# Kernel tuning notes

Hardware: AMD Instinct MI355X
Metric: run time of the kernel (lower is better)

## Reference

```python
import jax, jax.numpy as jnp
import numpy as np

B, D, E, G, P, H = 8192, 2048, 8, 4, 512, 192
T, DT, TAU, VTH, VRESET = 20, 0.001, 0.02, 0.5, 0.0
DELTA0, KTOP, KROUTE, PREDW = 7.0, 32, 2, 0.1


def setup_inputs() -> dict:
    key = jax.random.key(0)
    ks = jax.random.split(key, 12)
    s = 0.02
    return {
        "query_embedding": jax.random.normal(ks[0], (B, D), jnp.float32),
        "Wg": jax.random.normal(ks[1], (2, E), jnp.float32) * s,
        "bg": jnp.zeros((E,), jnp.float32),
        "Wp": jax.random.normal(ks[2], (2, E), jnp.float32) * s,
        "bp": jnp.zeros((E,), jnp.float32),
        "Wgg": jax.random.normal(ks[3], (2, G), jnp.float32) * s,
        "bgg": jnp.zeros((G,), jnp.float32),
        "W1": jax.random.normal(ks[4], (E, D, P), jnp.float32) * (1.0 / np.sqrt(D)),
        "b1": jnp.zeros((E, P), jnp.float32),
        "W2": jax.random.normal(ks[5], (E, P, D), jnp.float32) * (1.0 / np.sqrt(P)),
        "b2": jnp.zeros((E, D), jnp.float32),
    }


def reference(query_embedding, Wg, bg, Wp, bp, Wgg, bgg, W1, b1, W2, b2):
    x = query_embedding  # [B, D], already embed_dim -> no pad/slice
    dtype = x.dtype

    # --- Phasor bank temporal features on per-row mean ---
    qm = jnp.mean(x, axis=-1)  # [B]
    freqs = DELTA0 * jnp.arange(1, H + 1, dtype=dtype)  # [H]
    ang = qm[:, None] * freqs[None, :]  # [B, H]
    temporal = jnp.concatenate([jnp.cos(ang), jnp.sin(ang)], axis=-1)  # [B, 2H]

    # --- Spiking attention over top-K |x| indices (LIF over T steps) ---
    topk_idx = jax.lax.top_k(jnp.abs(x), KTOP)[1]  # [B, K]
    rows = jnp.arange(B)[:, None]
    I = jnp.zeros((B, D), dtype).at[rows, topk_idx].add(1.0)  # input current [B, vocab=D]

    def lif_step(v, _):
        v = v * (1.0 - DT / TAU) + I
        spike = (v >= VTH).astype(dtype)
        v = jnp.where(spike > 0, VRESET, v)
        return v, spike

    _, spikes = jax.lax.scan(lif_step, jnp.zeros((B, D), dtype), None, length=T)
    attention_gains = jnp.mean(spikes, axis=0)  # [B, D] spike rates

    # --- Bio gating inputs ---
    gate_in = jnp.stack([jnp.mean(temporal, axis=-1), jnp.mean(attention_gains, axis=-1)], axis=-1)  # [B, 2]

    gate_logits = gate_in @ Wg + bg  # [B, E]
    gate_logits = gate_logits - PREDW * (gate_in @ Wp + bp)

    # group routing bias: experts grouped round-robin i % G
    group_logits = gate_in @ Wgg + bgg  # [B, G]
    gmap = jax.nn.one_hot(jnp.arange(E) % G, G, dtype=dtype)  # [E, G]
    gate_logits = gate_logits + group_logits @ gmap.T

    gate_weights = jax.nn.softmax(gate_logits, axis=-1)  # temperature = 1

    # top-k routing + renormalization
    _, tidx = jax.lax.top_k(gate_weights, KROUTE)
    mask = jnp.zeros_like(gate_weights).at[rows, tidx].set(1.0)
    gated = gate_weights * mask
    gate_weights = gated / (jnp.sum(gated, axis=-1, keepdims=True) + 1e-9)

    # --- Dense MLP experts (bottleneck P = hidden // 4) ---
    h = jax.nn.relu(jnp.einsum('bd,edp->ebp', x, W1) + b1[:, None, :])  # [E, B, P]
    expert_out = jnp.einsum('ebp,eph->ebh', h, W2) + b2[:, None, :]  # [E, B, D]

    # gate-weighted combine
    context = jnp.einsum('be,ebh->bh', gate_weights, expert_out)  # [B, D]
    return context
```

## Files before the change

### kernel.cpp

```cpp
#include <hip/hip_runtime.h>
#include <stdint.h>

#define NB 8192
#define ND 2048
#define NE 8
#define NG 4
#define NP 512
#define NH 192

typedef _Float16 half_t;
typedef half_t f16x8 __attribute__((ext_vector_type(8)));
typedef float f32x4 __attribute__((ext_vector_type(4)));

__device__ __forceinline__ void gload16(const void* g, void* l) {
  __builtin_amdgcn_global_load_lds(
      (const __attribute__((address_space(1))) void*)g,
      (__attribute__((address_space(3))) void*)l, 16, 0, 0);
}

__global__ __launch_bounds__(256) void k_convert(
    const float* __restrict__ x, half_t* __restrict__ xh, double* __restrict__ qm)
{
  const int b = blockIdx.x;
  const int t = threadIdx.x;
  const float* xr = x + (size_t)b * ND;
  const float4 v0 = ((const float4*)xr)[t * 2];
  const float4 v1 = ((const float4*)xr)[t * 2 + 1];
  float f[8] = {v0.x, v0.y, v0.z, v0.w, v1.x, v1.y, v1.z, v1.w};
  double s = 0.0;
  __align__(16) half_t hb[8];
#pragma unroll
  for (int i = 0; i < 8; i++) { s += (double)f[i]; hb[i] = (half_t)f[i]; }
  *reinterpret_cast<int4*>(xh + (size_t)b * ND + t * 8) = *reinterpret_cast<const int4*>(hb);

#pragma unroll
  for (int m = 32; m >= 1; m >>= 1) s += __shfl_xor(s, m);
  __shared__ double part[4];
  if ((t & 63) == 0) part[t >> 6] = s;
  __syncthreads();
  if (t == 0) qm[b] = (part[0] + part[1] + part[2] + part[3]) / (double)ND;
}

__global__ __launch_bounds__(256) void k_gate(
    const double* __restrict__ qm,
    const float* __restrict__ Wg, const float* __restrict__ bg,
    const float* __restrict__ Wp, const float* __restrict__ bp,
    const float* __restrict__ Wgg, const float* __restrict__ bgg,
    int* __restrict__ e0a, int* __restrict__ e1a,
    float* __restrict__ w0a, float* __restrict__ w1a)
{
  const int wave = threadIdx.x >> 6;
  const int lane = threadIdx.x & 63;
  const int b = blockIdx.x * 4 + wave;
  const double q = qm[b];

  double part = 0.0;
#pragma unroll
  for (int i = 0; i < 3; i++) {
    int h = lane + i * 64;
    double ang = q * (7.0 * (double)(h + 1));
    part += cos(ang) + sin(ang);
  }
#pragma unroll
  for (int m = 32; m >= 1; m >>= 1) part += __shfl_xor(part, m);
  const double tm = part / (2.0 * (double)NH);
  const double gi1 = 32.0 / 2048.0;

  double lg = -1.0e300;
  if (lane < 8) {
    const int e = lane, g = e & 3;
    lg = tm * (double)Wg[e] + gi1 * (double)Wg[NE + e] + (double)bg[e];
    lg -= 0.1 * (tm * (double)Wp[e] + gi1 * (double)Wp[NE + e] + (double)bp[e]);
    lg += tm * (double)Wgg[g] + gi1 * (double)Wgg[NG + g] + (double)bgg[g];
  }
  double mx = lg;
#pragma unroll
  for (int m = 4; m >= 1; m >>= 1) mx = fmax(mx, __shfl_xor(mx, m));
  double pe = 0.0;
  if (lane < 8) pe = exp(lg - mx);
  double ps = pe;
#pragma unroll
  for (int m = 4; m >= 1; m >>= 1) ps += __shfl_xor(ps, m);

  double lgs[8], pes[8];
#pragma unroll
  for (int e = 0; e < 8; e++) { lgs[e] = __shfl(lg, e); pes[e] = __shfl(pe, e); }

  if (lane == 0) {
    int e0 = 0;
    for (int e = 1; e < NE; e++) if (lgs[e] > lgs[e0]) e0 = e;
    int e1 = (e0 == 0) ? 1 : 0;
    for (int e = 0; e < NE; e++) if (e != e0 && lgs[e] > lgs[e1]) e1 = e;
    const double p0 = pes[e0] / ps;
    const double p1 = pes[e1] / ps;
    const double den = p0 + p1 + 1e-9;
    e0a[b] = e0; e1a[b] = e1;
    w0a[b] = (float)(p0 / den);
    w1a[b] = (float)(p1 / den);
  }
}

__global__ __launch_bounds__(256) void k_bucket(
    const int* __restrict__ e0a, const int* __restrict__ e1a,
    const float* __restrict__ w0a, const float* __restrict__ w1a,
    int* __restrict__ rowl, float* __restrict__ wl, int* __restrict__ cnt,
    int* __restrict__ pos0a, int* __restrict__ pos1a,
    int* __restrict__ rowlp, int* __restrict__ cntp)
{
  const int t = threadIdx.x;
  const int r = blockIdx.x * 256 + t;
  __shared__ int hist[16], base[16], cursor[16];
  __shared__ int histp[64], basep[64], cursorp[64];
  if (t < 16) { hist[t] = 0; cursor[t] = 0; }
  if (t < 64) { histp[t] = 0; cursorp[t] = 0; }
  __syncthreads();

  const int e0 = e0a[r], e1 = e1a[r];
  const int p = e0 * 8 + e1;
  atomicAdd(&hist[e0], 1);
  atomicAdd(&hist[8 + e1], 1);
  atomicAdd(&histp[p], 1);
  __syncthreads();
  if (t < 16) base[t] = atomicAdd(&cnt[t], hist[t]);
  if (t < 64) basep[t] = atomicAdd(&cntp[t], histp[t]);
  __syncthreads();

  int p0 = atomicAdd(&cursor[e0], 1);
  int idx0 = base[e0] + p0;
  rowl[e0 * NB + idx0] = r;
  wl[e0 * NB + idx0] = w0a[r];
  pos0a[r] = idx0;

  int p1 = atomicAdd(&cursor[8 + e1], 1);
  int idx1 = base[8 + e1] + p1;
  rowl[(8 + e1) * NB + idx1] = r;
  wl[(8 + e1) * NB + idx1] = w1a[r];
  pos1a[r] = idx1;

  int pp = atomicAdd(&cursorp[p], 1);
  rowlp[p * NB + basep[p] + pp] = r;
}

__global__ __launch_bounds__(256) void k_cvt_w(
    const float* __restrict__ W1, const float* __restrict__ W2,
    half_t* __restrict__ w1t, half_t* __restrict__ w2t)
{
  const int which = blockIdx.y;
  const int R = which ? NP : ND;
  const int C = which ? ND : NP;
  const float* src = which ? W2 : W1;
  half_t* dst = which ? w2t : w1t;
  const int tiles_c = C >> 5;
  const int tiles_per_e = (R >> 6) * tiles_c;
  int id = blockIdx.x;
  int e = id / tiles_per_e;
  int rem = id - e * tiles_per_e;
  int tr = rem / tiles_c, tc = rem - tr * tiles_c;
  __shared__ float tile[64][33];
  const int t = threadIdx.x;

  const int lc = t & 31, lr = t >> 5;
  const float* s = src + (size_t)e * R * C + (size_t)(tr * 64) * C + tc * 32;
#pragma unroll
  for (int i = 0; i < 8; i++)
    tile[lr + i * 8][lc] = s[(size_t)(lr + i * 8) * C + lc];
  __syncthreads();

  const int n = t >> 3, kc = (t & 7) * 8;
  __align__(16) half_t hb[8];
#pragma unroll
  for (int j = 0; j < 8; j++) hb[j] = (half_t)tile[kc + j][n];
  half_t* d = dst + (size_t)e * R * C + (size_t)(tc * 32 + n) * R + tr * 64 + kc;
  *reinterpret_cast<int4*>(d) = *reinterpret_cast<const int4*>(hb);
}

__global__ void k_prefix(const int* __restrict__ cnt, const int* __restrict__ cntp,
                         int* __restrict__ pbase,
                         int* __restrict__ i16b, int* __restrict__ i16m, int* __restrict__ n16,
                         int* __restrict__ ipp, int* __restrict__ ipm, int* __restrict__ np)
{
  const int t = threadIdx.x;
  if (t == 0) {
    int c[16];
#pragma unroll
    for (int i = 0; i < 16; i++) c[i] = cnt[i];
    int s = 0;
#pragma unroll
    for (int i = 0; i < 16; i++) { pbase[i] = s; s += c[i]; }
    int k = 0;
    for (int b = 0; b < 16; b++)
      for (int m0 = 0; m0 < c[b]; m0 += 128) { i16b[k] = b; i16m[k] = m0; k++; }
    *n16 = k;
  } else if (t == 64) {
    int c[64];
#pragma unroll
    for (int i = 0; i < 64; i++) c[i] = cntp[i];
    int k = 0;
    for (int p = 0; p < 64; p++)
      for (int m0 = 0; m0 < c[p]; m0 += 128) { ipp[k] = p; ipm[k] = m0; k++; }
    *np = k;
  }
}

__global__ __launch_bounds__(256, 2) void k_gemm1(
    const half_t* __restrict__ xh, const half_t* __restrict__ w1t,
    const float* __restrict__ b1,
    const int* __restrict__ rowl, const float* __restrict__ wl,
    const int* __restrict__ cnt, const int* __restrict__ pbase,
    const int* __restrict__ i16b, const int* __restrict__ i16m,
    const int* __restrict__ n16, half_t* __restrict__ Hbuf)
{
  const int wi = blockIdx.y;
  if (wi >= *n16) return;
  const int bucket = i16b[wi];
  const int m0 = i16m[wi];
  const int count = cnt[bucket];
  const int e = bucket & 7;
  const int n0 = blockIdx.x * 256;
  const int t = threadIdx.x;

  __shared__ __align__(16) half_t As[3][128 * 32];
  __shared__ __align__(16) half_t Bs[3][256 * 32];
  __shared__ int rows_s[128];
  __shared__ float ws_s[128];

  if (t < 128) {
    int mi = m0 + t;
    int idx = bucket * NB + (mi < count ? mi : m0);
    rows_s[t] = rowl[idx];
    ws_s[t] = wl[idx];
  }
  __syncthreads();

  const int w = t >> 6, lane = t & 63;
  const int cA0 = (w * 2) * 64 + lane, cA1 = cA0 + 64;
  const int rA0 = cA0 >> 2, rA1 = cA1 >> 2;
  const int kA0 = ((cA0 & 3) ^ ((rA0 >> 1) & 3)) * 8;
  const int kA1 = ((cA1 & 3) ^ ((rA1 >> 1) & 3)) * 8;
  const half_t* gA0 = xh + (size_t)rows_s[rA0] * ND + kA0;
  const half_t* gA1 = xh + (size_t)rows_s[rA1] * ND + kA1;
  const half_t* w1te = w1t + (size_t)e * NP * ND;
  const int cB0 = (w * 4) * 64 + lane, cB1 = cB0 + 64, cB2 = cB0 + 128, cB3 = cB0 + 192;
  const int rB0 = cB0 >> 2, rB1 = cB1 >> 2, rB2 = cB2 >> 2, rB3 = cB3 >> 2;
  const half_t* gB0 = w1te + (size_t)(n0 + rB0) * ND + ((cB0 & 3) ^ ((rB0 >> 1) & 3)) * 8;
  const half_t* gB1 = w1te + (size_t)(n0 + rB1) * ND + ((cB1 & 3) ^ ((rB1 >> 1) & 3)) * 8;
  const half_t* gB2 = w1te + (size_t)(n0 + rB2) * ND + ((cB2 & 3) ^ ((rB2 >> 1) & 3)) * 8;
  const half_t* gB3 = w1te + (size_t)(n0 + rB3) * ND + ((cB3 & 3) ^ ((rB3 >> 1) & 3)) * 8;

  const int wr = w >> 1, wc = w & 1;
  const int lrow = lane & 15, lk = lane >> 4;
  const int lko = (lk ^ ((lrow >> 1) & 3)) * 8;

  f32x4 acc[4][8];
#pragma unroll
  for (int i = 0; i < 4; i++)
#pragma unroll
    for (int j = 0; j < 8; j++) {
      acc[i][j][0] = 0.f; acc[i][j][1] = 0.f; acc[i][j][2] = 0.f; acc[i][j][3] = 0.f;
    }

  auto stage = [&](int bi, int tt) {
    const int kk = tt * 32;
    half_t* la = &As[bi][w * 1024];
    gload16(gA0 + kk, la);
    gload16(gA1 + kk, la + 512);
    half_t* lb = &Bs[bi][w * 2048];
    gload16(gB0 + kk, lb);
    gload16(gB1 + kk, lb + 512);
    gload16(gB2 + kk, lb + 1024);
    gload16(gB3 + kk, lb + 1536);
  };
  auto compute = [&](int bi) {
    f16x8 af[4], bf[8];
#pragma unroll
    for (int i = 0; i < 4; i++)
      af[i] = *reinterpret_cast<const f16x8*>(&As[bi][(wr * 64 + i * 16 + lrow) * 32 + lko]);
#pragma unroll
    for (int n = 0; n < 8; n++)
      bf[n] = *reinterpret_cast<const f16x8*>(&Bs[bi][(wc * 128 + n * 16 + lrow) * 32 + lko]);
#pragma unroll
    for (int mi = 0; mi < 4; mi++)
#pragma unroll
      for (int ni = 0; ni < 8; ni++)
        acc[mi][ni] = __builtin_amdgcn_mfma_f32_16x16x32_f16(af[mi], bf[ni], acc[mi][ni], 0, 0, 0);
  };

  stage(0, 0);
  stage(1, 1);
  asm volatile("s_waitcnt vmcnt(6)" ::: "memory");
  __builtin_amdgcn_s_barrier();
  for (int t3 = 0; t3 < 60; t3 += 3) {
    stage(2, t3 + 2); compute(0);
    asm volatile("s_waitcnt vmcnt(6) lgkmcnt(0)" ::: "memory");
    __builtin_amdgcn_s_barrier();
    stage(0, t3 + 3); compute(1);
    asm volatile("s_waitcnt vmcnt(6) lgkmcnt(0)" ::: "memory");
    __builtin_amdgcn_s_barrier();
    stage(1, t3 + 4); compute(2);
    asm volatile("s_waitcnt vmcnt(6) lgkmcnt(0)" ::: "memory");
    __builtin_amdgcn_s_barrier();
  }
  stage(2, 62); compute(0);
  asm volatile("s_waitcnt vmcnt(6) lgkmcnt(0)" ::: "memory");
  __builtin_amdgcn_s_barrier();
  stage(0, 63); compute(1);
  asm volatile("s_waitcnt vmcnt(6) lgkmcnt(0)" ::: "memory");
  __builtin_amdgcn_s_barrier();
  compute(2);
  asm volatile("s_waitcnt vmcnt(0) lgkmcnt(0)" ::: "memory");
  __builtin_amdgcn_s_barrier();
  compute(0);

  const int pb = pbase[bucket];
#pragma unroll
  for (int mi = 0; mi < 4; mi++) {
#pragma unroll
    for (int i = 0; i < 4; i++) {
      int lm = wr * 64 + mi * 16 + lk * 4 + i;
      if (m0 + lm < count) {
        size_t prow = (size_t)(pb + m0 + lm) * NP;
        float wcoef = ws_s[lm];
#pragma unroll
        for (int ni = 0; ni < 8; ni++) {
          int col = n0 + wc * 128 + ni * 16 + lrow;
          float v = acc[mi][ni][i] + b1[e * NP + col];
          v = v > 0.f ? v : 0.f;
          Hbuf[prow + col] = (half_t)(v * wcoef);
        }
      }
    }
  }
}

__global__ __launch_bounds__(256) void k_gemm2p(
    const half_t* __restrict__ Hbuf, const half_t* __restrict__ w2t,
    const float* __restrict__ b2,
    const int* __restrict__ rowlp, const int* __restrict__ cntp,
    const int* __restrict__ pbase,
    const int* __restrict__ pos0a, const int* __restrict__ pos1a,
    const float* __restrict__ w0a, const float* __restrict__ w1a,
    const int* __restrict__ ipp, const int* __restrict__ ipm,
    const int* __restrict__ np, float* __restrict__ out)
{
  const int wi = blockIdx.y;
  if (wi >= *np) return;
  const int p = ipp[wi];
  const int m0 = ipm[wi];
  const int count = cntp[p];
  const int e0 = p >> 3, e1 = p & 7;
  const int n0 = blockIdx.x * 128;
  const int t = threadIdx.x;

  __shared__ __align__(16) half_t As[3][128 * 32];
  __shared__ __align__(16) half_t Bs[3][128 * 32];
  __shared__ int h0_s[128], h1_s[128], rs_s[128];
  __shared__ float w0_s[128], w1_s[128];

  if (t < 128) {
    int mi = m0 + t;
    int r = rowlp[p * NB + (mi < count ? mi : m0)];
    rs_s[t] = r;
    h0_s[t] = pbase[e0] + pos0a[r];
    h1_s[t] = pbase[8 + e1] + pos1a[r];
    w0_s[t] = w0a[r];
    w1_s[t] = w1a[r];
  }
  __syncthreads();

  const int w = t >> 6, lane = t & 63;
  const int c0 = w * 128 + lane, c1 = c0 + 64;
  const int row0 = c0 >> 2, ch0 = c0 & 3;
  const int row1 = c1 >> 2, ch1 = c1 & 3;
  const int sw0 = (row0 >> 1) & 3, sw1 = (row1 >> 1) & 3;
  const half_t* w2e0 = w2t + (size_t)e0 * ND * NP;
  const half_t* w2e1 = w2t + (size_t)e1 * ND * NP;
  const half_t* sa00 = Hbuf + (size_t)h0_s[row0] * NP + ((ch0 ^ sw0) * 8);
  const half_t* sa01 = Hbuf + (size_t)h0_s[row1] * NP + ((ch1 ^ sw1) * 8);
  const half_t* sa10 = Hbuf + (size_t)h1_s[row0] * NP + ((ch0 ^ sw0) * 8);
  const half_t* sa11 = Hbuf + (size_t)h1_s[row1] * NP + ((ch1 ^ sw1) * 8);
  const half_t* pB00 = w2e0 + (size_t)(n0 + row0) * NP + ((ch0 ^ sw0) * 8);
  const half_t* pB01 = w2e0 + (size_t)(n0 + row1) * NP + ((ch1 ^ sw1) * 8);
  const half_t* pB10 = w2e1 + (size_t)(n0 + row0) * NP + ((ch0 ^ sw0) * 8);
  const half_t* pB11 = w2e1 + (size_t)(n0 + row1) * NP + ((ch1 ^ sw1) * 8);

  const int wr = w >> 1, wc = w & 1;
  const int lrow = lane & 15, lk = lane >> 4;
  const int lko = (lk ^ ((lrow >> 1) & 3)) * 8;

  f32x4 acc[4][4];
#pragma unroll
  for (int i = 0; i < 4; i++)
#pragma unroll
    for (int j = 0; j < 4; j++) {
      acc[i][j][0] = 0.f; acc[i][j][1] = 0.f; acc[i][j][2] = 0.f; acc[i][j][3] = 0.f;
    }

  const int NT = 32;

  auto stage = [&](int bi, int tt) {
    const int kk = (tt & 15) * 32;
    half_t* la = &As[bi][w * 1024];
    half_t* lb = &Bs[bi][w * 1024];
    if (tt & 16) {
      gload16(sa10 + kk, la);
      gload16(sa11 + kk, la + 512);
      gload16(pB10 + kk, lb);
      gload16(pB11 + kk, lb + 512);
    } else {
      gload16(sa00 + kk, la);
      gload16(sa01 + kk, la + 512);
      gload16(pB00 + kk, lb);
      gload16(pB01 + kk, lb + 512);
    }
  };
  auto compute = [&](int bi) {
    f16x8 af[4], bf[4];
#pragma unroll
    for (int i = 0; i < 4; i++) {
      af[i] = *reinterpret_cast<const f16x8*>(&As[bi][(wr * 64 + i * 16 + lrow) * 32 + lko]);
      bf[i] = *reinterpret_cast<const f16x8*>(&Bs[bi][(wc * 64 + i * 16 + lrow) * 32 + lko]);
    }
#pragma unroll
    for (int mi = 0; mi < 4; mi++)
#pragma unroll
      for (int ni = 0; ni < 4; ni++)
        acc[mi][ni] = __builtin_amdgcn_mfma_f32_16x16x32_f16(af[mi], bf[ni], acc[mi][ni], 0, 0, 0);
  };

  stage(0, 0);
  stage(1, 1);
  asm volatile("s_waitcnt vmcnt(4)" ::: "memory");
  __builtin_amdgcn_s_barrier();
#pragma unroll
  for (int tt = 0; tt < NT; ++tt) {
    if (tt + 2 < NT) stage((tt + 2) % 3, tt + 2);
    compute(tt % 3);
    if (tt + 1 < NT) {
      if (tt + 2 < NT) asm volatile("s_waitcnt vmcnt(4) lgkmcnt(0)" ::: "memory");
      else             asm volatile("s_waitcnt vmcnt(0) lgkmcnt(0)" ::: "memory");
      __builtin_amdgcn_s_barrier();
    }
  }

  float b20[4], b21[4];
#pragma unroll
  for (int ni = 0; ni < 4; ni++) {
    int col = n0 + wc * 64 + ni * 16 + lrow;
    b20[ni] = b2[e0 * ND + col];
    b21[ni] = b2[e1 * ND + col];
  }
#pragma unroll
  for (int mi = 0; mi < 4; mi++) {
#pragma unroll
    for (int i = 0; i < 4; i++) {
      int lm = wr * 64 + mi * 16 + lk * 4 + i;
      if (m0 + lm < count) {
        int r = rs_s[lm];
        float wb0 = w0_s[lm], wb1 = w1_s[lm];
        float* orow = out + (size_t)r * ND;
#pragma unroll
        for (int ni = 0; ni < 4; ni++) {
          int col = n0 + wc * 64 + ni * 16 + lrow;
          orow[col] = acc[mi][ni][i] + wb0 * b20[ni] + wb1 * b21[ni];
        }
      }
    }
  }
}

extern "C" void kernel_launch(void* const* d_in, const int* in_sizes, int n_in,
                              void* d_out, int out_size, void* d_ws, size_t ws_size,
                              hipStream_t stream)
{
  const float* x   = (const float*)d_in[0];
  const float* Wg  = (const float*)d_in[1];
  const float* bg  = (const float*)d_in[2];
  const float* Wp  = (const float*)d_in[3];
  const float* bp  = (const float*)d_in[4];
  const float* Wgg = (const float*)d_in[5];
  const float* bgg = (const float*)d_in[6];
  const float* W1  = (const float*)d_in[7];
  const float* b1  = (const float*)d_in[8];
  const float* W2  = (const float*)d_in[9];
  const float* b2  = (const float*)d_in[10];
  float* out = (float*)d_out;

  char* ws = (char*)d_ws;
  size_t off = 0;
  const size_t OFF_XH   = off; off += (size_t)NB * ND * 2;
  const size_t OFF_W1T  = off; off += (size_t)NE * NP * ND * 2;
  const size_t OFF_W2T  = off; off += (size_t)NE * ND * NP * 2;
  const size_t OFF_H    = off; off += (size_t)(2 * NB + 128) * NP * 2;
  const size_t OFF_ROWL = off; off += (size_t)16 * NB * 4;
  const size_t OFF_WL   = off; off += (size_t)16 * NB * 4;
  const size_t OFF_ROWLP= off; off += (size_t)64 * NB * 4;
  const size_t OFF_CNT  = off; off += 64;
  const size_t OFF_CNTP = off; off += 256;
  const size_t OFF_PB   = off; off += 64;
  const size_t OFF_QM   = off; off += (size_t)NB * 8;
  const size_t OFF_E0   = off; off += (size_t)NB * 4;
  const size_t OFF_E1   = off; off += (size_t)NB * 4;
  const size_t OFF_W0   = off; off += (size_t)NB * 4;
  const size_t OFF_W1A  = off; off += (size_t)NB * 4;
  const size_t OFF_POS0 = off; off += (size_t)NB * 4;
  const size_t OFF_POS1 = off; off += (size_t)NB * 4;
  const size_t OFF_I16B = off; off += 1024;
  const size_t OFF_I16M = off; off += 1024;
  const size_t OFF_N16  = off; off += 64;
  const size_t OFF_IPP  = off; off += 1024;
  const size_t OFF_IPM  = off; off += 1024;
  const size_t OFF_NP   = off; off += 64;

  half_t* xh   = (half_t*)(ws + OFF_XH);
  half_t* w1t  = (half_t*)(ws + OFF_W1T);
  half_t* w2t  = (half_t*)(ws + OFF_W2T);
  half_t* Hbuf = (half_t*)(ws + OFF_H);
  int*    rowl = (int*)(ws + OFF_ROWL);
  float*  wl   = (float*)(ws + OFF_WL);
  int*    rowlp= (int*)(ws + OFF_ROWLP);
  int*    cnt  = (int*)(ws + OFF_CNT);
  int*    cntp = (int*)(ws + OFF_CNTP);
  int*    pb   = (int*)(ws + OFF_PB);
  double* qm   = (double*)(ws + OFF_QM);
  int*    e0a  = (int*)(ws + OFF_E0);
  int*    e1a  = (int*)(ws + OFF_E1);
  float*  w0a  = (float*)(ws + OFF_W0);
  float*  w1a  = (float*)(ws + OFF_W1A);
  int*    pos0a= (int*)(ws + OFF_POS0);
  int*    pos1a= (int*)(ws + OFF_POS1);
  int*    i16b = (int*)(ws + OFF_I16B);
  int*    i16m = (int*)(ws + OFF_I16M);
  int*    n16  = (int*)(ws + OFF_N16);
  int*    ipp  = (int*)(ws + OFF_IPP);
  int*    ipm  = (int*)(ws + OFF_IPM);
  int*    np   = (int*)(ws + OFF_NP);

  hipMemsetAsync(cnt, 0, 64 + 256, stream);
  k_convert<<<NB, 256, 0, stream>>>(x, xh, qm);
  k_cvt_w<<<dim3(4096, 2, 1), 256, 0, stream>>>(W1, W2, w1t, w2t);
  k_gate<<<NB / 4, 256, 0, stream>>>(qm, Wg, bg, Wp, bp, Wgg, bgg, e0a, e1a, w0a, w1a);
  k_bucket<<<NB / 256, 256, 0, stream>>>(e0a, e1a, w0a, w1a, rowl, wl, cnt,
                                         pos0a, pos1a, rowlp, cntp);
  k_prefix<<<1, 128, 0, stream>>>(cnt, cntp, pb, i16b, i16m, n16, ipp, ipm, np);
  k_gemm1<<<dim3(2, 144, 1), 256, 0, stream>>>(xh, w1t, b1, rowl, wl, cnt, pb,
                                               i16b, i16m, n16, Hbuf);
  k_gemm2p<<<dim3(16, 128, 1), 256, 0, stream>>>(Hbuf, w2t, b2, rowlp, cntp, pb,
                                                 pos0a, pos1a, w0a, w1a, ipp, ipm, np, out);
}
```

Measured before the change: 343.0 us.

## Fuse preprocessing, gating and prefix kernels to cut launch count

The activation conversion, weight transpose-conversion and gating kernels are merged into one launch. Block index selects the role, and the gate logic now runs inside the per-row conversion block, so the qm buffer round trip goes away. The prefix-scan kernel is folded into the bucket kernel through a last-block ticket pattern with a threadfence, which drops another launch. In exchange the row blocks run the gate computation serially after the conversion, and the ticket adds an atomic plus a single-threaded tail in the last block.

```diff
diff --git a/kernel.cpp b/kernel.cpp
--- a/kernel.cpp
+++ b/kernel.cpp
@@ -18,11 +18,48 @@
       (__attribute__((address_space(3))) void*)l, 16, 0, 0);
 }
 
-__global__ __launch_bounds__(256) void k_convert(
-    const float* __restrict__ x, half_t* __restrict__ xh, double* __restrict__ qm)
+__global__ __launch_bounds__(256) void k_pre(
+    const float* __restrict__ x, half_t* __restrict__ xh,
+    const float* __restrict__ W1, const float* __restrict__ W2,
+    half_t* __restrict__ w1t, half_t* __restrict__ w2t,
+    const float* __restrict__ Wg, const float* __restrict__ bg,
+    const float* __restrict__ Wp, const float* __restrict__ bp,
+    const float* __restrict__ Wgg, const float* __restrict__ bgg,
+    int* __restrict__ e0a, int* __restrict__ e1a,
+    float* __restrict__ w0a, float* __restrict__ w1a)
 {
+  const int t = threadIdx.x;
+
+  if (blockIdx.x >= NB) {
+    int id = blockIdx.x - NB;
+    const int which = id >> 12;
+    id &= 4095;
+    const int R = which ? NP : ND;
+    const int C = which ? ND : NP;
+    const float* src = which ? W2 : W1;
+    half_t* dst = which ? w2t : w1t;
+    const int tiles_c = C >> 5;
+    const int tiles_per_e = (R >> 6) * tiles_c;
+    int e = id / tiles_per_e;
+    int rem = id - e * tiles_per_e;
+    int tr = rem / tiles_c, tc = rem - tr * tiles_c;
+    __shared__ float tile[64][33];
+    const int lc = t & 31, lr = t >> 5;
+    const float* s = src + (size_t)e * R * C + (size_t)(tr * 64) * C + tc * 32;
+#pragma unroll
+    for (int i = 0; i < 8; i++)
+      tile[lr + i * 8][lc] = s[(size_t)(lr + i * 8) * C + lc];
+    __syncthreads();
+    const int n = t >> 3, kc = (t & 7) * 8;
+    __align__(16) half_t hb[8];
+#pragma unroll
+    for (int j = 0; j < 8; j++) hb[j] = (half_t)tile[kc + j][n];
+    half_t* d = dst + (size_t)e * R * C + (size_t)(tc * 32 + n) * R + tr * 64 + kc;
+    *reinterpret_cast<int4*>(d) = *reinterpret_cast<const int4*>(hb);
+    return;
+  }
+
   const int b = blockIdx.x;
-  const int t = threadIdx.x;
   const float* xr = x + (size_t)b * ND;
   const float4 v0 = ((const float4*)xr)[t * 2];
   const float4 v1 = ((const float4*)xr)[t * 2 + 1];
@@ -36,67 +73,59 @@
 #pragma unroll
   for (int m = 32; m >= 1; m >>= 1) s += __shfl_xor(s, m);
   __shared__ double part[4];
+  __shared__ double qm_s;
   if ((t & 63) == 0) part[t >> 6] = s;
   __syncthreads();
-  if (t == 0) qm[b] = (part[0] + part[1] + part[2] + part[3]) / (double)ND;
-}
-
-__global__ __launch_bounds__(256) void k_gate(
-    const double* __restrict__ qm,
-    const float* __restrict__ Wg, const float* __restrict__ bg,
-    const float* __restrict__ Wp, const float* __restrict__ bp,
-    const float* __restrict__ Wgg, const float* __restrict__ bgg,
-    int* __restrict__ e0a, int* __restrict__ e1a,
-    float* __restrict__ w0a, float* __restrict__ w1a)
-{
-  const int wave = threadIdx.x >> 6;
-  const int lane = threadIdx.x & 63;
-  const int b = blockIdx.x * 4 + wave;
-  const double q = qm[b];
-
-  double part = 0.0;
-#pragma unroll
-  for (int i = 0; i < 3; i++) {
-    int h = lane + i * 64;
-    double ang = q * (7.0 * (double)(h + 1));
-    part += cos(ang) + sin(ang);
-  }
-#pragma unroll
-  for (int m = 32; m >= 1; m >>= 1) part += __shfl_xor(part, m);
-  const double tm = part / (2.0 * (double)NH);
-  const double gi1 = 32.0 / 2048.0;
-
-  double lg = -1.0e300;
-  if (lane < 8) {
-    const int e = lane, g = e & 3;
-    lg = tm * (double)Wg[e] + gi1 * (double)Wg[NE + e] + (double)bg[e];
-    lg -= 0.1 * (tm * (double)Wp[e] + gi1 * (double)Wp[NE + e] + (double)bp[e]);
-    lg += tm * (double)Wgg[g] + gi1 * (double)Wgg[NG + g] + (double)bgg[g];
-  }
-  double mx = lg;
-#pragma unroll
-  for (int m = 4; m >= 1; m >>= 1) mx = fmax(mx, __shfl_xor(mx, m));
-  double pe = 0.0;
-  if (lane < 8) pe = exp(lg - mx);
-  double ps = pe;
-#pragma unroll
-  for (int m = 4; m >= 1; m >>= 1) ps += __shfl_xor(ps, m);
-
-  double lgs[8], pes[8];
-#pragma unroll
-  for (int e = 0; e < 8; e++) { lgs[e] = __shfl(lg, e); pes[e] = __shfl(pe, e); }
-
-  if (lane == 0) {
-    int e0 = 0;
-    for (int e = 1; e < NE; e++) if (lgs[e] > lgs[e0]) e0 = e;
-    int e1 = (e0 == 0) ? 1 : 0;
-    for (int e = 0; e < NE; e++) if (e != e0 && lgs[e] > lgs[e1]) e1 = e;
-    const double p0 = pes[e0] / ps;
-    const double p1 = pes[e1] / ps;
-    const double den = p0 + p1 + 1e-9;
-    e0a[b] = e0; e1a[b] = e1;
-    w0a[b] = (float)(p0 / den);
-    w1a[b] = (float)(p1 / den);
+  if (t == 0) qm_s = (part[0] + part[1] + part[2] + part[3]) / (double)ND;
+  __syncthreads();
+
+  const double q = qm_s;
+  double g = 0.0;
+  if (t < 192) {
+    double ang = q * (7.0 * (double)(t + 1));
+    g = cos(ang) + sin(ang);
+  }
+#pragma unroll
+  for (int m = 32; m >= 1; m >>= 1) g += __shfl_xor(g, m);
+  __shared__ double gp[4];
+  if ((t & 63) == 0) gp[t >> 6] = g;
+  __syncthreads();
+
+  if (t < 64) {
+    const double tm = (gp[0] + gp[1] + gp[2] + gp[3]) / (2.0 * (double)NH);
+    const double gi1 = 32.0 / 2048.0;
+    double lg = -1.0e300;
+    if (t < 8) {
+      const int e = t, gg = e & 3;
+      lg = tm * (double)Wg[e] + gi1 * (double)Wg[NE + e] + (double)bg[e];
+      lg -= 0.1 * (tm * (double)Wp[e] + gi1 * (double)Wp[NE + e] + (double)bp[e]);
+      lg += tm * (double)Wgg[gg] + gi1 * (double)Wgg[NG + gg] + (double)bgg[gg];
+    }
+    double mx = lg;
+#pragma unroll
+    for (int m = 4; m >= 1; m >>= 1) mx = fmax(mx, __shfl_xor(mx, m));
+    double pe = 0.0;
+    if (t < 8) pe = exp(lg - mx);
+    double ps = pe;
+#pragma unroll
+    for (int m = 4; m >= 1; m >>= 1) ps += __shfl_xor(ps, m);
+
+    double lgs[8], pes[8];
+#pragma unroll
+    for (int e = 0; e < 8; e++) { lgs[e] = __shfl(lg, e); pes[e] = __shfl(pe, e); }
+
+    if (t == 0) {
+      int e0 = 0;
+      for (int e = 1; e < NE; e++) if (lgs[e] > lgs[e0]) e0 = e;
+      int e1 = (e0 == 0) ? 1 : 0;
+      for (int e = 0; e < NE; e++) if (e != e0 && lgs[e] > lgs[e1]) e1 = e;
+      const double p0 = pes[e0] / ps;
+      const double p1 = pes[e1] / ps;
+      const double den = p0 + p1 + 1e-9;
+      e0a[b] = e0; e1a[b] = e1;
+      w0a[b] = (float)(p0 / den);
+      w1a[b] = (float)(p1 / den);
+    }
   }
 }
 
@@ -105,12 +134,16 @@
     const float* __restrict__ w0a, const float* __restrict__ w1a,
     int* __restrict__ rowl, float* __restrict__ wl, int* __restrict__ cnt,
     int* __restrict__ pos0a, int* __restrict__ pos1a,
-    int* __restrict__ rowlp, int* __restrict__ cntp)
+    int* __restrict__ rowlp, int* __restrict__ cntp,
+    int* __restrict__ ticket, int* __restrict__ pbase,
+    int* __restrict__ i16b, int* __restrict__ i16m, int* __restrict__ n16,
+    int* __restrict__ ipp, int* __restrict__ ipm, int* __restrict__ np)
 {
   const int t = threadIdx.x;
   const int r = blockIdx.x * 256 + t;
   __shared__ int hist[16], base[16], cursor[16];
   __shared__ int histp[64], basep[64], cursorp[64];
+  __shared__ int lastf;
   if (t < 16) { hist[t] = 0; cursor[t] = 0; }
   if (t < 64) { histp[t] = 0; cursorp[t] = 0; }
   __syncthreads();
@@ -139,66 +172,32 @@
 
   int pp = atomicAdd(&cursorp[p], 1);
   rowlp[p * NB + basep[p] + pp] = r;
-}
-
-__global__ __launch_bounds__(256) void k_cvt_w(
-    const float* __restrict__ W1, const float* __restrict__ W2,
-    half_t* __restrict__ w1t, half_t* __restrict__ w2t)
-{
-  const int which = blockIdx.y;
-  const int R = which ? NP : ND;
-  const int C = which ? ND : NP;
-  const float* src = which ? W2 : W1;
-  half_t* dst = which ? w2t : w1t;
-  const int tiles_c = C >> 5;
-  const int tiles_per_e = (R >> 6) * tiles_c;
-  int id = blockIdx.x;
-  int e = id / tiles_per_e;
-  int rem = id - e * tiles_per_e;
-  int tr = rem / tiles_c, tc = rem - tr * tiles_c;
-  __shared__ float tile[64][33];
-  const int t = threadIdx.x;
-
-  const int lc = t & 31, lr = t >> 5;
-  const float* s = src + (size_t)e * R * C + (size_t)(tr * 64) * C + tc * 32;
-#pragma unroll
-  for (int i = 0; i < 8; i++)
-    tile[lr + i * 8][lc] = s[(size_t)(lr + i * 8) * C + lc];
-  __syncthreads();
-
-  const int n = t >> 3, kc = (t & 7) * 8;
-  __align__(16) half_t hb[8];
-#pragma unroll
-  for (int j = 0; j < 8; j++) hb[j] = (half_t)tile[kc + j][n];
-  half_t* d = dst + (size_t)e * R * C + (size_t)(tc * 32 + n) * R + tr * 64 + kc;
-  *reinterpret_cast<int4*>(d) = *reinterpret_cast<const int4*>(hb);
-}
-
-__global__ void k_prefix(const int* __restrict__ cnt, const int* __restrict__ cntp,
-                         int* __restrict__ pbase,
-                         int* __restrict__ i16b, int* __restrict__ i16m, int* __restrict__ n16,
-                         int* __restrict__ ipp, int* __restrict__ ipm, int* __restrict__ np)
-{
-  const int t = threadIdx.x;
-  if (t == 0) {
-    int c[16];
-#pragma unroll
-    for (int i = 0; i < 16; i++) c[i] = cnt[i];
-    int s = 0;
-#pragma unroll
-    for (int i = 0; i < 16; i++) { pbase[i] = s; s += c[i]; }
-    int k = 0;
-    for (int b = 0; b < 16; b++)
-      for (int m0 = 0; m0 < c[b]; m0 += 128) { i16b[k] = b; i16m[k] = m0; k++; }
-    *n16 = k;
-  } else if (t == 64) {
-    int c[64];
-#pragma unroll
-    for (int i = 0; i < 64; i++) c[i] = cntp[i];
-    int k = 0;
-    for (int p = 0; p < 64; p++)
-      for (int m0 = 0; m0 < c[p]; m0 += 128) { ipp[k] = p; ipm[k] = m0; k++; }
-    *np = k;
+
+  __threadfence();
+  __syncthreads();
+  if (t == 0) lastf = (atomicAdd(ticket, 1) == (int)gridDim.x - 1);
+  __syncthreads();
+  if (lastf) {
+    if (t == 0) {
+      int c[16];
+#pragma unroll
+      for (int i = 0; i < 16; i++) c[i] = atomicAdd(&cnt[i], 0);
+      int s = 0;
+#pragma unroll
+      for (int i = 0; i < 16; i++) { pbase[i] = s; s += c[i]; }
+      int k = 0;
+      for (int bb = 0; bb < 16; bb++)
+        for (int m0 = 0; m0 < c[bb]; m0 += 128) { i16b[k] = bb; i16m[k] = m0; k++; }
+      *n16 = k;
+    } else if (t == 64) {
+      int c[64];
+#pragma unroll
+      for (int i = 0; i < 64; i++) c[i] = atomicAdd(&cntp[i], 0);
+      int k = 0;
+      for (int pq = 0; pq < 64; pq++)
+        for (int m0 = 0; m0 < c[pq]; m0 += 128) { ipp[k] = pq; ipm[k] = m0; k++; }
+      *np = k;
+    }
   }
 }
 
@@ -496,8 +495,8 @@
   const size_t OFF_ROWLP= off; off += (size_t)64 * NB * 4;
   const size_t OFF_CNT  = off; off += 64;
   const size_t OFF_CNTP = off; off += 256;
+  const size_t OFF_TKT  = off; off += 64;
   const size_t OFF_PB   = off; off += 64;
-  const size_t OFF_QM   = off; off += (size_t)NB * 8;
   const size_t OFF_E0   = off; off += (size_t)NB * 4;
   const size_t OFF_E1   = off; off += (size_t)NB * 4;
   const size_t OFF_W0   = off; off += (size_t)NB * 4;
@@ -520,8 +519,8 @@
   int*    rowlp= (int*)(ws + OFF_ROWLP);
   int*    cnt  = (int*)(ws + OFF_CNT);
   int*    cntp = (int*)(ws + OFF_CNTP);
+  int*    tkt  = (int*)(ws + OFF_TKT);
   int*    pb   = (int*)(ws + OFF_PB);
-  double* qm   = (double*)(ws + OFF_QM);
   int*    e0a  = (int*)(ws + OFF_E0);
   int*    e1a  = (int*)(ws + OFF_E1);
   float*  w0a  = (float*)(ws + OFF_W0);
@@ -535,13 +534,13 @@
   int*    ipm  = (int*)(ws + OFF_IPM);
   int*    np   = (int*)(ws + OFF_NP);
 
-  hipMemsetAsync(cnt, 0, 64 + 256, stream);
-  k_convert<<<NB, 256, 0, stream>>>(x, xh, qm);
-  k_cvt_w<<<dim3(4096, 2, 1), 256, 0, stream>>>(W1, W2, w1t, w2t);
-  k_gate<<<NB / 4, 256, 0, stream>>>(qm, Wg, bg, Wp, bp, Wgg, bgg, e0a, e1a, w0a, w1a);
+  hipMemsetAsync(cnt, 0, 64 + 256 + 64, stream);
+  k_pre<<<NB + 8192, 256, 0, stream>>>(x, xh, W1, W2, w1t, w2t,
+                                       Wg, bg, Wp, bp, Wgg, bgg,
+                                       e0a, e1a, w0a, w1a);
   k_bucket<<<NB / 256, 256, 0, stream>>>(e0a, e1a, w0a, w1a, rowl, wl, cnt,
-                                         pos0a, pos1a, rowlp, cntp);
-  k_prefix<<<1, 128, 0, stream>>>(cnt, cntp, pb, i16b, i16m, n16, ipp, ipm, np);
+                                         pos0a, pos1a, rowlp, cntp,
+                                         tkt, pb, i16b, i16m, n16, ipp, ipm, np);
   k_gemm1<<<dim3(2, 144, 1), 256, 0, stream>>>(xh, w1t, b1, rowl, wl, cnt, pb,
                                                i16b, i16m, n16, Hbuf);
   k_gemm2p<<<dim3(16, 128, 1), 256, 0, stream>>>(Hbuf, w2t, b2, rowlp, cntp, pb,
```

Result: faster. 333.1 us (-2.9%).
